# Kernel tuning notes

Measured on AMD Instinct MI355X. Metric: run time of the kernel, lower is better.

Reference implementation:

```python
import jax, jax.numpy as jnp
import numpy as np

# Fixed by module source: forward hardcodes a 200x200 BEV grid, dim=128,
# MSDeformAttn(n_levels=1, n_heads=4, n_points=8).
B, Z, X, C, H, P = 2, 200, 200, 128, 4, 8
N = Z * X
D = C // H  # head dim = 32


def setup_inputs() -> dict:
    key = jax.random.key(0)
    ks = jax.random.split(key, 12)
    s = 0.02
    return {
        "query": jax.random.normal(ks[0], (B, N, C), jnp.float32),
        # MSDeformAttn.value_proj
        "Wv": jax.random.normal(ks[1], (C, C), jnp.float32) * s,
        "bv": jnp.zeros((C,), jnp.float32),
        # MSDeformAttn.sampling_offsets (C -> H*1*P*2)
        "Woff": jax.random.normal(ks[2], (C, H * P * 2), jnp.float32) * s,
        "boff": jax.random.normal(ks[3], (H * P * 2,), jnp.float32) * 2.0,
        # MSDeformAttn.attention_weights (C -> H*1*P)
        "Wattn": jax.random.normal(ks[4], (C, H * P), jnp.float32) * s,
        "battn": jnp.zeros((H * P,), jnp.float32),
        # MSDeformAttn.output_proj
        "Wout1": jax.random.normal(ks[5], (C, C), jnp.float32) * s,
        "bout1": jnp.zeros((C,), jnp.float32),
        # VanillaSelfAttention.output_proj
        "Wout2": jax.random.normal(ks[6], (C, C), jnp.float32) * s,
        "bout2": jnp.zeros((C,), jnp.float32),
    }


def _forward(query, Wv, bv, Woff, boff, Wattn, battn, Wout1, bout1, Wout2, bout2):
    # Reference points: normalized centers of the 200x200 grid, order (z, x).
    zc = (jnp.arange(Z, dtype=jnp.float32) + 0.5) / Z
    xc = (jnp.arange(X, dtype=jnp.float32) + 0.5) / X
    ref = jnp.stack(jnp.meshgrid(zc, xc, indexing="ij"), axis=-1).reshape(N, 2)

    # value_proj on input_flatten (== query); split heads, lay out as images.
    value = (query @ Wv + bv).reshape(B, Z, X, H, D)
    value_flat = value.transpose(0, 3, 1, 2, 4).reshape(B * H, Z * X, D)  # (BH, ZX, D)

    # Sampling locations: ref + offsets / offset_normalizer ([W, H] = [200, 200]).
    off = (query @ Woff + boff).reshape(B, N, H, P, 2)
    norm = jnp.array([X, Z], jnp.float32)
    loc = ref[None, :, None, None, :] + off / norm  # (B, N, H, P, 2)

    # Attention weights: softmax over n_levels*n_points (= P here).
    attn = jax.nn.softmax((query @ Wattn + battn).reshape(B, N, H, P), axis=-1)

    # grid_sample convention: grid = 2*loc - 1, grid[...,0]=x (width), align_corners=False.
    grid = 2.0 * loc - 1.0
    ix = ((grid[..., 0] + 1.0) * X - 1.0) * 0.5  # pixel x coords
    iy = ((grid[..., 1] + 1.0) * Z - 1.0) * 0.5  # pixel y coords
    ix = ix.transpose(0, 2, 1, 3).reshape(B * H, N * P)
    iy = iy.transpose(0, 2, 1, 3).reshape(B * H, N * P)

    x0f = jnp.floor(ix); y0f = jnp.floor(iy)
    lx = ix - x0f; ly = iy - y0f
    x0 = x0f.astype(jnp.int32); y0 = y0f.astype(jnp.int32)
    x1 = x0 + 1; y1 = y0 + 1

    def corner(xi, yi, w):
        # zero padding: out-of-bounds corners contribute 0
        valid = (xi >= 0) & (xi < X) & (yi >= 0) & (yi < Z)
        idx = jnp.clip(yi, 0, Z - 1) * X + jnp.clip(xi, 0, X - 1)  # (BH, N*P)
        v = jnp.take_along_axis(value_flat, idx[..., None], axis=1)  # (BH, N*P, D)
        return v * (w * valid.astype(w.dtype))[..., None]

    sampled = (
        corner(x0, y0, (1.0 - lx) * (1.0 - ly))
        + corner(x1, y0, lx * (1.0 - ly))
        + corner(x0, y1, (1.0 - lx) * ly)
        + corner(x1, y1, lx * ly)
    ).reshape(B, H, N, P, D)

    # Weighted reduce over points, merge heads.
    out = jnp.einsum("bhnpd,bnhp->bnhd", sampled, attn).reshape(B, N, C)
    out = out @ Wout1 + bout1  # MSDeformAttn.output_proj
    out = out @ Wout2 + bout2  # VanillaSelfAttention.output_proj
    return out + query  # dropout is identity in eval; residual add


def reference(query, Wv, bv, Woff, boff, Wattn, battn, Wout1, bout1, Wout2, bout2):
    return _forward(query, Wv, bv, Woff, boff, Wattn, battn, Wout1, bout1, Wout2, bout2)
```

## Files before the change

kernel.cpp:

```cpp
#include <hip/hip_runtime.h>
#include <hip/hip_bf16.h>
#include <cstddef>

namespace {
constexpr int B  = 2;
constexpr int Z  = 200;
constexpr int X  = 200;
constexpr int C  = 128;
constexpr int H  = 4;
constexpr int P  = 8;
constexpr int N  = Z * X;
constexpr int BN = B * N;
constexpr int SC = 128;
constexpr int NF_P = 14;
constexpr int NF_O = 8;
constexpr int KS   = 4;

typedef __attribute__((ext_vector_type(8))) short short8;
typedef __attribute__((ext_vector_type(4))) float f32x4;
typedef _Float16 h16x2 __attribute__((ext_vector_type(2)));

__device__ inline ushort f2bf(float x) {
    __hip_bfloat16 h = __float2bfloat16(x);
    return *reinterpret_cast<ushort*>(&h);
}
__device__ inline unsigned packbf(float a, float b) {
    return (unsigned)f2bf(a) | ((unsigned)f2bf(b) << 16);
}
__device__ inline ushort f2h(float x) {
    _Float16 h = (_Float16)x;
    return __builtin_bit_cast(ushort, h);
}
__device__ inline float h1f(ushort u) {
    return (float)__builtin_bit_cast(_Float16, u);
}
__device__ inline float2 h2f2(unsigned u) {
    h16x2 h = __builtin_bit_cast(h16x2, u);
    return make_float2((float)h[0], (float)h[1]);
}
__device__ inline unsigned packh(float a, float b) {
    return (unsigned)f2h(a) | ((unsigned)f2h(b) << 16);
}
__device__ inline h16x2 pkrtz(float a, float b) {
    return __builtin_bit_cast(h16x2, __builtin_amdgcn_cvt_pkrtz(a, b));
}
template <int MASK>
__device__ inline float swzx(float x) {
    constexpr int pat = (MASK << 10) | 0x1F;
    return __int_as_float(__builtin_amdgcn_ds_swizzle(__float_as_int(x), pat));
}
template <int MASK>
__device__ inline h16x2 swzh(h16x2 x) {
    constexpr int pat = (MASK << 10) | 0x1F;
    int t = __builtin_amdgcn_ds_swizzle(__builtin_bit_cast(int, x), pat);
    return __builtin_bit_cast(h16x2, t);
}
}

__global__ __launch_bounds__(256) void vsa_k_prep(
    const float* __restrict__ Wv,    const float* __restrict__ bv,
    const float* __restrict__ Woff,  const float* __restrict__ boff,
    const float* __restrict__ Wattn, const float* __restrict__ battn,
    const float* __restrict__ Wout1, const float* __restrict__ bout1,
    const float* __restrict__ Wout2, const float* __restrict__ bout2,
    ushort* __restrict__ wtp, ushort* __restrict__ wtp2,
    float* __restrict__ biasp, float* __restrict__ bias2)
{
    const int u = blockIdx.x * 256 + threadIdx.x;
    constexpr int NP = KS * NF_P * 64;
    constexpr int NO = KS * NF_O * 64;

    if (u < NP) {
        int ks  = u / (NF_P * 64);
        int rem = u - ks * (NF_P * 64);
        int f = rem >> 6, l = rem & 63;
        int n  = f * 16 + (l & 15);
        int kb = ks * 32 + (l >> 4) * 8;
        float v[8];
        #pragma unroll
        for (int e = 0; e < 8; ++e) {
            int k = kb + e;
            if (n < 128)      v[e] = Wv[k * 128 + n];
            else if (n < 192) v[e] = Woff[k * 64 + (n - 128)];
            else              v[e] = Wattn[k * 32 + (n - 192)];
        }
        unsigned* dst = (unsigned*)(wtp + (size_t)u * 8);
        #pragma unroll
        for (int i = 0; i < 4; ++i) dst[i] = packbf(v[2*i], v[2*i+1]);
    } else if (u < NP + NO) {
        int t   = u - NP;
        int ks  = t / (NF_O * 64);
        int rem = t - ks * (NF_O * 64);
        int f = rem >> 6, l = rem & 63;
        int n  = f * 16 + (l & 15);
        int kb = ks * 32 + (l >> 4) * 8;
        float acc[8] = {0,0,0,0,0,0,0,0};
        for (int j = 0; j < 128; ++j) {
            float w2 = Wout2[j * 128 + n];
            #pragma unroll
            for (int e = 0; e < 8; ++e)
                acc[e] = fmaf(Wout1[(kb + e) * 128 + j], w2, acc[e]);
        }
        unsigned* dst = (unsigned*)(wtp2 + (size_t)t * 8);
        #pragma unroll
        for (int i = 0; i < 4; ++i) dst[i] = packh(acc[2*i], acc[2*i+1]);
    } else if (u < NP + NO + 224) {
        int c = u - NP - NO;
        float bb;
        if (c < 128)      bb = bv[c];
        else if (c < 192) bb = boff[c - 128];
        else              bb = battn[c - 192];
        biasp[c] = bb;
    } else if (u < NP + NO + 224 + 128) {
        int c = u - NP - NO - 224;
        float acc = bout2[c];
        for (int j = 0; j < 128; ++j)
            acc = fmaf(bout1[j], Wout2[j * 128 + c], acc);
        bias2[c] = acc;
    }
}

__global__ __launch_bounds__(256) void vsa_k_proj(
    const float* __restrict__ Q, const ushort* __restrict__ wtp,
    const float* __restrict__ biasp,
    ushort* __restrict__ proj_v16, ushort* __restrict__ proj_s16)
{
    const int lane = threadIdx.x & 63;
    const int wave = blockIdx.x * 4 + (threadIdx.x >> 6);
    const int row0 = wave * 16;
    const int m  = lane & 15;
    const int kg = lane >> 4;

    const float* qp = Q + (size_t)(row0 + m) * 128 + kg * 8;

    f32x4 acc[NF_P];
    #pragma unroll
    for (int f = 0; f < NF_P; ++f) acc[f] = (f32x4){0.f, 0.f, 0.f, 0.f};

    #pragma unroll
    for (int ks = 0; ks < KS; ++ks) {
        float4 a0 = *(const float4*)(qp + ks * 32);
        float4 a1 = *(const float4*)(qp + ks * 32 + 4);
        short8 af;
        af[0] = (short)f2bf(a0.x); af[1] = (short)f2bf(a0.y);
        af[2] = (short)f2bf(a0.z); af[3] = (short)f2bf(a0.w);
        af[4] = (short)f2bf(a1.x); af[5] = (short)f2bf(a1.y);
        af[6] = (short)f2bf(a1.z); af[7] = (short)f2bf(a1.w);
        const short8* wrow = (const short8*)wtp + ks * NF_P * 64 + lane;
        #pragma unroll
        for (int f = 0; f < NF_P; ++f)
            acc[f] = __builtin_amdgcn_mfma_f32_16x16x32_bf16(af, wrow[f * 64], acc[f], 0, 0, 0);
    }

    #pragma unroll
    for (int f = 0; f < 8; ++f) {
        const int col = f * 16 + m;
        const float bb = biasp[col];
        #pragma unroll
        for (int r = 0; r < 4; ++r)
            proj_v16[(size_t)(row0 + kg * 4 + r) * 128 + col] = f2h(acc[f][r] + bb);
    }
    #pragma unroll
    for (int f = 8; f < 12; ++f) {
        const int col = f * 16 + m;
        const float bb = biasp[col];
        const int c  = col - 128;
        const int hp = c >> 1, comp = c & 1;
        #pragma unroll
        for (int r = 0; r < 4; ++r)
            proj_s16[(size_t)(row0 + kg * 4 + r) * SC + hp * 4 + comp] = f2h(acc[f][r] + bb);
    }
    #pragma unroll
    for (int f = 12; f < 14; ++f) {
        const float bb = biasp[f * 16 + m];
        const int hp = (f - 12) * 16 + m;
        #pragma unroll
        for (int r = 0; r < 4; ++r) {
            float v = acc[f][r] + bb;
            float mx = v;
            mx = fmaxf(mx, swzx<1>(mx));
            mx = fmaxf(mx, swzx<2>(mx));
            mx = fmaxf(mx, swzx<4>(mx));
            float ex = __expf(v - mx);
            float sm = ex;
            sm += swzx<1>(sm); sm += swzx<2>(sm); sm += swzx<4>(sm);
            const float wp = ex / sm;
            proj_s16[(size_t)(row0 + kg * 4 + r) * SC + hp * 4 + 2] = f2h(wp);
        }
    }
}

__global__ __launch_bounds__(256) void vsa_k_sample(
    const ushort* __restrict__ proj_v16, const ushort* __restrict__ proj_s16,
    ushort* __restrict__ tmp)
{
    const int lane  = threadIdx.x & 63;
    const int w     = threadIdx.x >> 6;
    const int pixb  = w >> 1;
    const int hpair = w & 1;
    const int h     = hpair * 2 + (lane >> 5);
    const int p     = (lane >> 2) & 7;
    const int d8    = lane & 3;

    const int orig = blockIdx.x;
    const int wg   = (orig & 7) * 5000 + (orig >> 3);
    const int b    = wg / 20000;
    const int r2   = wg - b * 20000;
    const int j    = r2 / 100;
    const int i    = (r2 - j * 100) * 2 + pixb;
    const int bn   = b * N + i * X + j;

    const uint2 ow = *(const uint2*)(proj_s16 + (size_t)bn * SC + (h * 8 + p) * 4);
    const float2 off = h2f2(ow.x);
    const float  wp  = h1f((ushort)(ow.y & 0xffff));

    const float ixf = (float)i + off.x;
    const float iyf = (float)j + off.y;
    const float x0f = floorf(ixf), y0f = floorf(iyf);
    const float lx = ixf - x0f, ly = iyf - y0f;
    const int x0 = (int)x0f, y0 = (int)y0f;
    const int x1 = x0 + 1,  y1 = y0 + 1;
    const int xc0 = min(max(x0, 0), X - 1), xc1 = min(max(x1, 0), X - 1);
    const int yc0 = min(max(y0, 0), Z - 1), yc1 = min(max(y1, 0), Z - 1);

    const float wx0 = ((unsigned)x0 < (unsigned)X) ? (1.f - lx) : 0.f;
    const float wx1 = ((unsigned)x1 < (unsigned)X) ? lx : 0.f;
    const float wy0 = (((unsigned)y0 < (unsigned)Z) ? (1.f - ly) : 0.f) * wp;
    const float wy1 = (((unsigned)y1 < (unsigned)Z) ? ly : 0.f) * wp;

    const h16x2 w00p = pkrtz(wx0 * wy0, wx0 * wy0);
    const h16x2 w10p = pkrtz(wx1 * wy0, wx1 * wy0);
    const h16x2 w01p = pkrtz(wx0 * wy1, wx0 * wy1);
    const h16x2 w11p = pkrtz(wx1 * wy1, wx1 * wy1);

    const ushort* vb = proj_v16 + (size_t)b * N * 128;
    const int rb0 = yc0 * X, rb1 = yc1 * X;
    const int hb  = h * 32 + d8 * 8;

    const uint4 c00 = *(const uint4*)(vb + (size_t)(rb0 + xc0) * 128 + hb);
    const uint4 c10 = *(const uint4*)(vb + (size_t)(rb0 + xc1) * 128 + hb);
    const uint4 c01 = *(const uint4*)(vb + (size_t)(rb1 + xc0) * 128 + hb);
    const uint4 c11 = *(const uint4*)(vb + (size_t)(rb1 + xc1) * 128 + hb);

    h16x2 a0 = (h16x2)0, a1 = (h16x2)0, a2 = (h16x2)0, a3 = (h16x2)0;
    #define VSA_ACC(c, wpk) { \
        a0 = __builtin_elementwise_fma(__builtin_bit_cast(h16x2, (c).x), wpk, a0); \
        a1 = __builtin_elementwise_fma(__builtin_bit_cast(h16x2, (c).y), wpk, a1); \
        a2 = __builtin_elementwise_fma(__builtin_bit_cast(h16x2, (c).z), wpk, a2); \
        a3 = __builtin_elementwise_fma(__builtin_bit_cast(h16x2, (c).w), wpk, a3); }
    VSA_ACC(c00, w00p)
    VSA_ACC(c10, w10p)
    VSA_ACC(c01, w01p)
    VSA_ACC(c11, w11p)
    #undef VSA_ACC

    a0 += swzh<4>(a0);  a1 += swzh<4>(a1);  a2 += swzh<4>(a2);  a3 += swzh<4>(a3);
    a0 += swzh<8>(a0);  a1 += swzh<8>(a1);  a2 += swzh<8>(a2);  a3 += swzh<8>(a3);
    a0 += swzh<16>(a0); a1 += swzh<16>(a1); a2 += swzh<16>(a2); a3 += swzh<16>(a3);

    if (p == 0) {
        uint4 o;
        o.x = __builtin_bit_cast(unsigned, a0);
        o.y = __builtin_bit_cast(unsigned, a1);
        o.z = __builtin_bit_cast(unsigned, a2);
        o.w = __builtin_bit_cast(unsigned, a3);
        *(uint4*)(tmp + (size_t)bn * 128 + h * 32 + d8 * 8) = o;
    }
}

__global__ __launch_bounds__(256) void vsa_k_out(
    const ushort* __restrict__ tmp, const ushort* __restrict__ wtp2,
    const float* __restrict__ bias2, const float* __restrict__ Q,
    float* __restrict__ out)
{
    const int lane = threadIdx.x & 63;
    const int wave = blockIdx.x * 4 + (threadIdx.x >> 6);
    const int row0 = wave * 16;
    const int m  = lane & 15;
    const int kg = lane >> 4;

    const ushort* ap = tmp + (size_t)(row0 + m) * 128 + kg * 8;

    f32x4 acc[NF_O];
    #pragma unroll
    for (int f = 0; f < NF_O; ++f) acc[f] = (f32x4){0.f, 0.f, 0.f, 0.f};

    #pragma unroll
    for (int ks = 0; ks < KS; ++ks) {
        short8 af = *(const short8*)(ap + ks * 32);
        const short8* wrow = (const short8*)wtp2 + ks * NF_O * 64 + lane;
        #pragma unroll
        for (int f = 0; f < NF_O; ++f)
            acc[f] = __builtin_amdgcn_mfma_f32_16x16x32_f16(af, wrow[f * 64], acc[f], 0, 0, 0);
    }

    #pragma unroll
    for (int f = 0; f < NF_O; ++f) {
        const int col = f * 16 + m;
        const float bb = bias2[col];
        #pragma unroll
        for (int r = 0; r < 4; ++r) {
            const int row = row0 + kg * 4 + r;
            out[(size_t)row * 128 + col] = acc[f][r] + bb + Q[(size_t)row * 128 + col];
        }
    }
}

extern "C" void kernel_launch(void* const* d_in, const int* in_sizes, int n_in,
                              void* d_out, int out_size, void* d_ws, size_t ws_size,
                              hipStream_t stream) {
    const float* Q     = (const float*)d_in[0];
    const float* Wv    = (const float*)d_in[1];
    const float* bv    = (const float*)d_in[2];
    const float* Woff  = (const float*)d_in[3];
    const float* boff  = (const float*)d_in[4];
    const float* Wattn = (const float*)d_in[5];
    const float* battn = (const float*)d_in[6];
    const float* Wout1 = (const float*)d_in[7];
    const float* bout1 = (const float*)d_in[8];
    const float* Wout2 = (const float*)d_in[9];
    const float* bout2 = (const float*)d_in[10];
    float* out = (float*)d_out;

    float*  biasp  = (float*)d_ws;
    float*  bias2  = biasp + 224;
    ushort* proj_s16 = (ushort*)(bias2 + 128);
    ushort* proj_v16 = proj_s16 + (size_t)BN * SC;
    ushort* tmp    = proj_v16 + (size_t)BN * 128;
    ushort* wtp    = tmp + (size_t)BN * 128;
    ushort* wtp2   = wtp + (size_t)KS * NF_P * 64 * 8;

    constexpr int prep_n = KS * NF_P * 64 + KS * NF_O * 64 + 224 + 128;
    vsa_k_prep<<<(prep_n + 255) / 256, 256, 0, stream>>>(
        Wv, bv, Woff, boff, Wattn, battn, Wout1, bout1, Wout2, bout2,
        wtp, wtp2, biasp, bias2);
    vsa_k_proj<<<BN / 64, 256, 0, stream>>>(Q, wtp, biasp, proj_v16, proj_s16);
    vsa_k_sample<<<dim3((Z / 2) * X * B), 256, 0, stream>>>(proj_v16, proj_s16, tmp);
    vsa_k_out<<<BN / 64, 256, 0, stream>>>(tmp, wtp2, bias2, Q, out);
}
```

Before: 94.81 us.

## Fuse deformable sampling and output projection into one kernel via LDS

Merges the sampling kernel and the output-projection GEMM kernel. Each 256-thread block now samples 16 consecutive pixels into a shared-memory tile, then each wave runs MFMAs for two output column fragments and adds bias plus residual. This drops the global tmp buffer round trip and one kernel launch. The cost is a different sampling block mapping (16 pixels along a row instead of a 2-pixel column pair), which may change cache locality, and re-reading the weight fragments per 16-row block. Q loads and output stores are also switched to nontemporal.

```diff
diff --git a/kernel.cpp b/kernel.cpp
--- a/kernel.cpp
+++ b/kernel.cpp
@@ -190,118 +190,122 @@
     }
 }
 
-__global__ __launch_bounds__(256) void vsa_k_sample(
+__global__ __launch_bounds__(256) void vsa_k_so(
     const ushort* __restrict__ proj_v16, const ushort* __restrict__ proj_s16,
-    ushort* __restrict__ tmp)
+    const ushort* __restrict__ wtp2, const float* __restrict__ bias2,
+    const float* __restrict__ Q, float* __restrict__ out)
 {
-    const int lane  = threadIdx.x & 63;
-    const int w     = threadIdx.x >> 6;
-    const int pixb  = w >> 1;
-    const int hpair = w & 1;
-    const int h     = hpair * 2 + (lane >> 5);
-    const int p     = (lane >> 2) & 7;
-    const int d8    = lane & 3;
+    __shared__ ushort tmp_lds[16][136];
+
+    const int lane = threadIdx.x & 63;
+    const int wv   = threadIdx.x >> 6;
+    const int hsub = lane >> 5;
+    const int p    = (lane >> 2) & 7;
+    const int d8   = lane & 3;
 
     const int orig = blockIdx.x;
-    const int wg   = (orig & 7) * 5000 + (orig >> 3);
-    const int b    = wg / 20000;
-    const int r2   = wg - b * 20000;
-    const int j    = r2 / 100;
-    const int i    = (r2 - j * 100) * 2 + pixb;
-    const int bn   = b * N + i * X + j;
-
-    const uint2 ow = *(const uint2*)(proj_s16 + (size_t)bn * SC + (h * 8 + p) * 4);
-    const float2 off = h2f2(ow.x);
-    const float  wp  = h1f((ushort)(ow.y & 0xffff));
-
-    const float ixf = (float)i + off.x;
-    const float iyf = (float)j + off.y;
-    const float x0f = floorf(ixf), y0f = floorf(iyf);
-    const float lx = ixf - x0f, ly = iyf - y0f;
-    const int x0 = (int)x0f, y0 = (int)y0f;
-    const int x1 = x0 + 1,  y1 = y0 + 1;
-    const int xc0 = min(max(x0, 0), X - 1), xc1 = min(max(x1, 0), X - 1);
-    const int yc0 = min(max(y0, 0), Z - 1), yc1 = min(max(y1, 0), Z - 1);
-
-    const float wx0 = ((unsigned)x0 < (unsigned)X) ? (1.f - lx) : 0.f;
-    const float wx1 = ((unsigned)x1 < (unsigned)X) ? lx : 0.f;
-    const float wy0 = (((unsigned)y0 < (unsigned)Z) ? (1.f - ly) : 0.f) * wp;
-    const float wy1 = (((unsigned)y1 < (unsigned)Z) ? ly : 0.f) * wp;
-
-    const h16x2 w00p = pkrtz(wx0 * wy0, wx0 * wy0);
-    const h16x2 w10p = pkrtz(wx1 * wy0, wx1 * wy0);
-    const h16x2 w01p = pkrtz(wx0 * wy1, wx0 * wy1);
-    const h16x2 w11p = pkrtz(wx1 * wy1, wx1 * wy1);
+    const int wg   = (orig & 7) * 625 + (orig >> 3);
+    const int b    = wg / 2500;
+    const int bl0  = (wg - b * 2500) * 16;
+    const int i0   = bl0 / 200;
+    const int j0   = bl0 - i0 * 200;
+    const int bn0  = b * N + bl0;
 
     const ushort* vb = proj_v16 + (size_t)b * N * 128;
-    const int rb0 = yc0 * X, rb1 = yc1 * X;
-    const int hb  = h * 32 + d8 * 8;
-
-    const uint4 c00 = *(const uint4*)(vb + (size_t)(rb0 + xc0) * 128 + hb);
-    const uint4 c10 = *(const uint4*)(vb + (size_t)(rb0 + xc1) * 128 + hb);
-    const uint4 c01 = *(const uint4*)(vb + (size_t)(rb1 + xc0) * 128 + hb);
-    const uint4 c11 = *(const uint4*)(vb + (size_t)(rb1 + xc1) * 128 + hb);
-
-    h16x2 a0 = (h16x2)0, a1 = (h16x2)0, a2 = (h16x2)0, a3 = (h16x2)0;
-    #define VSA_ACC(c, wpk) { \
-        a0 = __builtin_elementwise_fma(__builtin_bit_cast(h16x2, (c).x), wpk, a0); \
-        a1 = __builtin_elementwise_fma(__builtin_bit_cast(h16x2, (c).y), wpk, a1); \
-        a2 = __builtin_elementwise_fma(__builtin_bit_cast(h16x2, (c).z), wpk, a2); \
-        a3 = __builtin_elementwise_fma(__builtin_bit_cast(h16x2, (c).w), wpk, a3); }
-    VSA_ACC(c00, w00p)
-    VSA_ACC(c10, w10p)
-    VSA_ACC(c01, w01p)
-    VSA_ACC(c11, w11p)
-    #undef VSA_ACC
-
-    a0 += swzh<4>(a0);  a1 += swzh<4>(a1);  a2 += swzh<4>(a2);  a3 += swzh<4>(a3);
-    a0 += swzh<8>(a0);  a1 += swzh<8>(a1);  a2 += swzh<8>(a2);  a3 += swzh<8>(a3);
-    a0 += swzh<16>(a0); a1 += swzh<16>(a1); a2 += swzh<16>(a2); a3 += swzh<16>(a3);
-
-    if (p == 0) {
-        uint4 o;
-        o.x = __builtin_bit_cast(unsigned, a0);
-        o.y = __builtin_bit_cast(unsigned, a1);
-        o.z = __builtin_bit_cast(unsigned, a2);
-        o.w = __builtin_bit_cast(unsigned, a3);
-        *(uint4*)(tmp + (size_t)bn * 128 + h * 32 + d8 * 8) = o;
-    }
-}
-
-__global__ __launch_bounds__(256) void vsa_k_out(
-    const ushort* __restrict__ tmp, const ushort* __restrict__ wtp2,
-    const float* __restrict__ bias2, const float* __restrict__ Q,
-    float* __restrict__ out)
-{
-    const int lane = threadIdx.x & 63;
-    const int wave = blockIdx.x * 4 + (threadIdx.x >> 6);
-    const int row0 = wave * 16;
+
+    #pragma unroll
+    for (int t = 0; t < 8; ++t) {
+        const int unit = t * 4 + wv;
+        const int pix  = unit >> 1;
+        const int h    = (unit & 1) * 2 + hsub;
+        const int jr   = j0 + pix;
+        const bool wr  = jr >= 200;
+        const int i    = i0 + (wr ? 1 : 0);
+        const int j    = wr ? jr - 200 : jr;
+        const int bn   = bn0 + pix;
+
+        const uint2 ow = *(const uint2*)(proj_s16 + (size_t)bn * SC + (h * 8 + p) * 4);
+        const float2 off = h2f2(ow.x);
+        const float  wp  = h1f((ushort)(ow.y & 0xffff));
+
+        const float ixf = (float)i + off.x;
+        const float iyf = (float)j + off.y;
+        const float x0f = floorf(ixf), y0f = floorf(iyf);
+        const float lx = ixf - x0f, ly = iyf - y0f;
+        const int x0 = (int)x0f, y0 = (int)y0f;
+        const int x1 = x0 + 1,  y1 = y0 + 1;
+        const int xc0 = min(max(x0, 0), X - 1), xc1 = min(max(x1, 0), X - 1);
+        const int yc0 = min(max(y0, 0), Z - 1), yc1 = min(max(y1, 0), Z - 1);
+
+        const float wx0 = ((unsigned)x0 < (unsigned)X) ? (1.f - lx) : 0.f;
+        const float wx1 = ((unsigned)x1 < (unsigned)X) ? lx : 0.f;
+        const float wy0 = (((unsigned)y0 < (unsigned)Z) ? (1.f - ly) : 0.f) * wp;
+        const float wy1 = (((unsigned)y1 < (unsigned)Z) ? ly : 0.f) * wp;
+
+        const h16x2 w00p = pkrtz(wx0 * wy0, wx0 * wy0);
+        const h16x2 w10p = pkrtz(wx1 * wy0, wx1 * wy0);
+        const h16x2 w01p = pkrtz(wx0 * wy1, wx0 * wy1);
+        const h16x2 w11p = pkrtz(wx1 * wy1, wx1 * wy1);
+
+        const int rb0 = yc0 * X, rb1 = yc1 * X;
+        const int hb  = h * 32 + d8 * 8;
+
+        const uint4 c00 = *(const uint4*)(vb + (size_t)(rb0 + xc0) * 128 + hb);
+        const uint4 c10 = *(const uint4*)(vb + (size_t)(rb0 + xc1) * 128 + hb);
+        const uint4 c01 = *(const uint4*)(vb + (size_t)(rb1 + xc0) * 128 + hb);
+        const uint4 c11 = *(const uint4*)(vb + (size_t)(rb1 + xc1) * 128 + hb);
+
+        h16x2 a0 = (h16x2)0, a1 = (h16x2)0, a2 = (h16x2)0, a3 = (h16x2)0;
+        #define VSA_ACC(c, wpk) { \
+            a0 = __builtin_elementwise_fma(__builtin_bit_cast(h16x2, (c).x), wpk, a0); \
+            a1 = __builtin_elementwise_fma(__builtin_bit_cast(h16x2, (c).y), wpk, a1); \
+            a2 = __builtin_elementwise_fma(__builtin_bit_cast(h16x2, (c).z), wpk, a2); \
+            a3 = __builtin_elementwise_fma(__builtin_bit_cast(h16x2, (c).w), wpk, a3); }
+        VSA_ACC(c00, w00p)
+        VSA_ACC(c10, w10p)
+        VSA_ACC(c01, w01p)
+        VSA_ACC(c11, w11p)
+        #undef VSA_ACC
+
+        a0 += swzh<4>(a0);  a1 += swzh<4>(a1);  a2 += swzh<4>(a2);  a3 += swzh<4>(a3);
+        a0 += swzh<8>(a0);  a1 += swzh<8>(a1);  a2 += swzh<8>(a2);  a3 += swzh<8>(a3);
+        a0 += swzh<16>(a0); a1 += swzh<16>(a1); a2 += swzh<16>(a2); a3 += swzh<16>(a3);
+
+        if (p == 0) {
+            uint4 o;
+            o.x = __builtin_bit_cast(unsigned, a0);
+            o.y = __builtin_bit_cast(unsigned, a1);
+            o.z = __builtin_bit_cast(unsigned, a2);
+            o.w = __builtin_bit_cast(unsigned, a3);
+            *(uint4*)(&tmp_lds[pix][h * 32 + d8 * 8]) = o;
+        }
+    }
+    __syncthreads();
+
     const int m  = lane & 15;
     const int kg = lane >> 4;
-
-    const ushort* ap = tmp + (size_t)(row0 + m) * 128 + kg * 8;
-
-    f32x4 acc[NF_O];
-    #pragma unroll
-    for (int f = 0; f < NF_O; ++f) acc[f] = (f32x4){0.f, 0.f, 0.f, 0.f};
-
+    const int f0 = wv * 2;
+
+    f32x4 acc0 = (f32x4){0.f, 0.f, 0.f, 0.f};
+    f32x4 acc1 = (f32x4){0.f, 0.f, 0.f, 0.f};
     #pragma unroll
     for (int ks = 0; ks < KS; ++ks) {
-        short8 af = *(const short8*)(ap + ks * 32);
+        short8 af = *(const short8*)(&tmp_lds[m][ks * 32 + kg * 8]);
         const short8* wrow = (const short8*)wtp2 + ks * NF_O * 64 + lane;
-        #pragma unroll
-        for (int f = 0; f < NF_O; ++f)
-            acc[f] = __builtin_amdgcn_mfma_f32_16x16x32_f16(af, wrow[f * 64], acc[f], 0, 0, 0);
-    }
-
-    #pragma unroll
-    for (int f = 0; f < NF_O; ++f) {
-        const int col = f * 16 + m;
+        acc0 = __builtin_amdgcn_mfma_f32_16x16x32_f16(af, wrow[f0 * 64], acc0, 0, 0, 0);
+        acc1 = __builtin_amdgcn_mfma_f32_16x16x32_f16(af, wrow[(f0 + 1) * 64], acc1, 0, 0, 0);
+    }
+
+    #pragma unroll
+    for (int ff = 0; ff < 2; ++ff) {
+        const int col = (f0 + ff) * 16 + m;
         const float bb = bias2[col];
         #pragma unroll
         for (int r = 0; r < 4; ++r) {
-            const int row = row0 + kg * 4 + r;
-            out[(size_t)row * 128 + col] = acc[f][r] + bb + Q[(size_t)row * 128 + col];
+            const float av = ff ? acc1[r] : acc0[r];
+            const size_t gi = (size_t)(bn0 + kg * 4 + r) * 128 + col;
+            const float q = __builtin_nontemporal_load(Q + gi);
+            __builtin_nontemporal_store(av + bb + q, out + gi);
         }
     }
 }
@@ -326,8 +330,7 @@
     float*  bias2  = biasp + 224;
     ushort* proj_s16 = (ushort*)(bias2 + 128);
     ushort* proj_v16 = proj_s16 + (size_t)BN * SC;
-    ushort* tmp    = proj_v16 + (size_t)BN * 128;
-    ushort* wtp    = tmp + (size_t)BN * 128;
+    ushort* wtp    = proj_v16 + (size_t)BN * 128;
     ushort* wtp2   = wtp + (size_t)KS * NF_P * 64 * 8;
 
     constexpr int prep_n = KS * NF_P * 64 + KS * NF_O * 64 + 224 + 128;
@@ -335,6 +338,5 @@
         Wv, bv, Woff, boff, Wattn, battn, Wout1, bout1, Wout2, bout2,
         wtp, wtp2, biasp, bias2);
     vsa_k_proj<<<BN / 64, 256, 0, stream>>>(Q, wtp, biasp, proj_v16, proj_s16);
-    vsa_k_sample<<<dim3((Z / 2) * X * B), 256, 0, stream>>>(proj_v16, proj_s16, tmp);
-    vsa_k_out<<<BN / 64, 256, 0, stream>>>(tmp, wtp2, bias2, Q, out);
-}
+    vsa_k_so<<<BN / 16, 256, 0, stream>>>(proj_v16, proj_s16, wtp2, bias2, Q, out);
+}
```

Result: no change. 95.82 us (+1.1%).
